# Kernel optimization log

Hardware: AMD Instinct MI355X
Metric: run time of the kernel (lower is better)

## Reference

```python
import jax, jax.numpy as jnp
import numpy as np

POS_DIM, COND_DIM, VIEW_DIM, HID = 3, 64, 3, 128
N_DENSITY, N_COLOR, SKIP = 8, 3, 4
DIN = POS_DIM + COND_DIM            # 67, density input dim
CIN = HID + VIEW_DIM                # 131, color input dim


def setup_inputs() -> dict:
    key = jax.random.key(0)
    ks = iter(jax.random.split(key, 64))

    def w(shape):
        return jax.random.normal(next(ks), shape, dtype=jnp.float32) * 0.05

    inp = {
        "pos": jax.random.normal(next(ks), (2048, 128, POS_DIM), dtype=jnp.float32),
        "cond": jax.random.normal(next(ks), (COND_DIM,), dtype=jnp.float32),
        "view": jax.random.normal(next(ks), (2048, VIEW_DIM), dtype=jnp.float32),
    }
    # density trunk: layer 0 takes DIN; layer SKIP+1 takes HID+DIN (skip concat); rest HID
    d_ins = [DIN] + [HID + DIN if i == SKIP + 1 else HID for i in range(1, N_DENSITY)]
    for i, din in enumerate(d_ins):
        inp[f"dW{i}"] = w((din, HID))
        inp[f"db{i}"] = w((HID,))
    inp["sW"], inp["sb"] = w((HID, 1)), w((1,))
    # color trunk
    c_ins = [CIN] + [HID // 2] * (N_COLOR - 1)
    for i, cin in enumerate(c_ins):
        inp[f"cW{i}"] = w((cin, HID // 2))
        inp[f"cb{i}"] = w((HID // 2,))
    inp["rW"], inp["rb"] = w((HID // 2, 3)), w((3,))
    return inp


def reference(pos, cond, view,
              dW0, db0, dW1, db1, dW2, db2, dW3, db3,
              dW4, db4, dW5, db5, dW6, db6, dW7, db7,
              sW, sb, cW0, cb0, cW1, cb1, cW2, cb2, rW, rb):
    bs, n_sample, _ = pos.shape
    cond_e = jnp.broadcast_to(cond[None, None, :], (bs, n_sample, COND_DIM))
    view_e = jnp.broadcast_to(view[:, None, :], (bs, n_sample, VIEW_DIM))

    x0 = jnp.concatenate([pos, cond_e], axis=-1)  # [bs, n, DIN]
    dWs = [dW0, dW1, dW2, dW3, dW4, dW5, dW6, dW7]
    dbs = [db0, db1, db2, db3, db4, db5, db6, db7]

    h = x0
    for i in range(N_DENSITY):
        h = jax.nn.relu(h @ dWs[i] + dbs[i])
        if i == SKIP:
            h = jnp.concatenate([x0, h], axis=-1)  # skip concat, input first
    sigma = h @ sW + sb  # [bs, n, 1]

    h = jnp.concatenate([h, view_e], axis=-1)  # [bs, n, CIN]
    cWs, cbs = [cW0, cW1, cW2], [cb0, cb1, cb2]
    for i in range(N_COLOR):
        h = jax.nn.relu(h @ cWs[i] + cbs[i])
    rgb = h @ rW + rb  # [bs, n, 3]

    return jnp.concatenate([rgb, sigma], axis=-1)  # [bs, n, 4]
```

## Files before the change

kernel.cpp:

```cpp
#include <hip/hip_runtime.h>

typedef _Float16 f16;
typedef _Float16 f16x8 __attribute__((ext_vector_type(8)));
typedef float f32x4 __attribute__((ext_vector_type(4)));

#define WS_PARAMS 262144

struct Ptrs { const float* p[29]; };

__device__ __forceinline__ int klogf(int q) {
  return ((q >> 5) << 5) | (((q >> 2) & 1) << 4) | (((q >> 3) & 3) << 2) | (q & 3);
}

__global__ void nerf_prep(Ptrs ptrs, char* __restrict__ ws) {
  const int t = threadIdx.x;
  if (blockIdx.x == 0) {
    float* P = (float*)(ws + WS_PARAMS);
    const float* cond = ptrs.p[1];
    const float* dW0 = ptrs.p[3];  const float* db0 = ptrs.p[4];
    const float* dW5 = ptrs.p[13]; const float* db5 = ptrs.p[14];
    if (t < 128) {
      float a0 = db0[t], a5 = db5[t];
      for (int k = 0; k < 64; ++k) {
        const float c = cond[k];
        a0 += c * dW0[(3 + k) * 128 + t];
        a5 += c * dW5[(3 + k) * 128 + t];
      }
      P[t] = a0;
      P[512 + t] = a5;
      for (int k = 0; k < 3; ++k) {
        P[128 + k * 128 + t] = dW0[k * 128 + t];
        P[640 + k * 128 + t] = dW5[k * 128 + t];
      }
      P[1024 + t] = ptrs.p[6][t];
      P[1152 + t] = ptrs.p[8][t];
      P[1280 + t] = ptrs.p[10][t];
      P[1408 + t] = ptrs.p[12][t];
      P[1536 + t] = ptrs.p[16][t];
      P[1664 + t] = ptrs.p[18][t];
      P[2176 + t] = ptrs.p[19][t];
    }
    if (t < 64) {
      P[1792 + t] = ptrs.p[22][t];
      for (int k = 0; k < 3; ++k)
        P[1856 + k * 64 + t] = ptrs.p[21][(128 + k) * 64 + t];
      P[2048 + t] = ptrs.p[24][t];
      P[2112 + t] = ptrs.p[26][t];
      for (int c = 0; c < 3; ++c)
        P[2308 + c * 64 + t] = ptrs.p[27][t * 3 + c];
    }
    if (t == 0) {
      P[2304] = ptrs.p[20][0];
      P[2500] = ptrs.p[28][0];
      P[2501] = ptrs.p[28][1];
      P[2502] = ptrs.p[28][2];
    }
    if (t < 3)  P[2305 + t] = 0.f;
    if (t < 57) P[2503 + t] = 0.f;
    return;
  }
  const int e = (blockIdx.x - 1) * 256 + t;
  float v; int dst;
  if (e < 114688) {
    const int img = e >> 14, o = e & 16383;
    const int j = o & 7, lane = (o >> 3) & 63, ks = (o >> 9) & 3, T = o >> 11;
    const int kraw = ks * 32 + ((lane >> 4) << 3) + j;
    const int k = (img == 0) ? kraw : klogf(kraw);
    const int ch = T * 16 + (lane & 15);
    v = ptrs.p[5 + 2 * img][(k + (img == 4 ? 67 : 0)) * 128 + ch];
    dst = img * 32768 + (((T * 4 + ks) * 64 + lane) << 4) + (j << 1);
  } else if (e < 122880) {
    const int o = e - 114688;
    const int j = o & 7, lane = (o >> 3) & 63, ks = (o >> 9) & 3, T = o >> 11;
    const int k = klogf(ks * 32 + ((lane >> 4) << 3) + j);
    const int ch = T * 16 + (lane & 15);
    v = ptrs.p[21][k * 64 + ch];
    dst = 229376 + (((T * 4 + ks) * 64 + lane) << 4) + (j << 1);
  } else if (e < 126976) {
    const int o = e - 122880;
    const int j = o & 7, lane = (o >> 3) & 63, ks = (o >> 9) & 1, T = o >> 10;
    const int k = klogf(ks * 32 + ((lane >> 4) << 3) + j);
    const int ch = T * 16 + (lane & 15);
    v = ptrs.p[23][k * 64 + ch];
    dst = 245760 + (((T * 2 + ks) * 64 + lane) << 4) + (j << 1);
  } else {
    const int o = e - 126976;
    const int j = o & 7, lane = (o >> 3) & 63, ks = (o >> 9) & 1, T = o >> 10;
    const int k = klogf(ks * 32 + ((lane >> 4) << 3) + j);
    const int ch = T * 16 + (lane & 15);
    v = ptrs.p[25][k * 64 + ch];
    dst = 253952 + (((T * 2 + ks) * 64 + lane) << 4) + (j << 1);
  }
  *(f16*)(ws + dst) = (f16)v;
}

__device__ __forceinline__ void loadF4(f16x8* A, const char* __restrict__ img,
                                       int fragBase, int lane) {
#pragma unroll
  for (int i = 0; i < 4; ++i)
    A[i] = *(const f16x8*)(img + (((fragBase + i) * 64 + lane) << 4));
}

template<int HCT, int NKS, int INIT, int CTBASE>
__device__ __forceinline__ void qL(const f16x8 B[4][4], f32x4 acc[4][8],
                                   const f16x8* A,
                                   const float* __restrict__ P,
                                   const float px[4][3],
                                   const float* __restrict__ vw2,
                                   int biasOff, int kg, int wbase) {
#pragma unroll
  for (int ct = 0; ct < HCT; ++ct) {
    const int ochB = (CTBASE + ct) * 16 + kg * 4;
    const f32x4 bq = *(const f32x4*)(P + biasOff + ochB);
    f32x4 e0, e1, e2;
    if (INIT == 1) {
      e0 = *(const f32x4*)(P + 640 + ochB);
      e1 = *(const f32x4*)(P + 768 + ochB);
      e2 = *(const f32x4*)(P + 896 + ochB);
    } else if (INIT == 2) {
      e0 = *(const f32x4*)(P + 1856 + ochB);
      e1 = *(const f32x4*)(P + 1920 + ochB);
      e2 = *(const f32x4*)(P + 1984 + ochB);
    }
#pragma unroll
    for (int ptc = 0; ptc < 4; ++ptc) {
      f32x4 v = bq;
      if (INIT == 1)
        v += px[ptc][0] * e0 + px[ptc][1] * e1 + px[ptc][2] * e2;
      if (INIT == 2) {
        const int ray = (wbase + ptc * 16) >> 7;
        v += vw2[ray * 3] * e0 + vw2[ray * 3 + 1] * e1 + vw2[ray * 3 + 2] * e2;
      }
      acc[ptc][CTBASE + ct] = v;
    }
  }
  __builtin_amdgcn_s_setprio(1);
#pragma unroll
  for (int ct = 0; ct < HCT; ++ct)
#pragma unroll
    for (int ks = 0; ks < NKS; ++ks)
#pragma unroll
      for (int ptc = 0; ptc < 4; ++ptc)
        acc[ptc][CTBASE + ct] = __builtin_amdgcn_mfma_f32_16x16x32_f16(
            A[ct * NKS + ks], B[ptc][ks], acc[ptc][CTBASE + ct], 0, 0, 0);
  __builtin_amdgcn_s_setprio(0);
}

template<int NCT>
__device__ __forceinline__ void toB(const f32x4 acc[4][8], f16x8 B[4][4]) {
#pragma unroll
  for (int ptc = 0; ptc < 4; ++ptc)
#pragma unroll
    for (int ks = 0; ks < NCT / 2; ++ks) {
      f16x8 hb;
#pragma unroll
      for (int r = 0; r < 4; ++r) {
        hb[r]     = (f16)fmaxf(acc[ptc][2 * ks][r], 0.f);
        hb[4 + r] = (f16)fmaxf(acc[ptc][2 * ks + 1][r], 0.f);
      }
      B[ptc][ks] = hb;
    }
}

__global__ __launch_bounds__(512, 2) void nerf_main(
    const float* __restrict__ pos, const float* __restrict__ view,
    const char* __restrict__ ws, float* __restrict__ out) {
  __shared__ __align__(16) float Lp[2560 + 1536 + 16];
  const int t = threadIdx.x, lane = t & 63, w = t >> 6;
  const int c = lane & 15, kg = lane >> 4;
  const int base = blockIdx.x * 512;
  const int wbase = w * 64;
  const float* P = Lp;
  float* Lpos = Lp + 2560;
  float* Lvw = Lp + 4096;

  for (int i = t; i < 2560; i += 512) Lp[i] = ((const float*)(ws + WS_PARAMS))[i];
  for (int i = t; i < 1536; i += 512) Lpos[i] = pos[base * 3 + i];
  if (t < 12) Lvw[t] = view[(base >> 7) * 3 + t];
  __syncthreads();

  f16x8 Aa[4], Ab[4];
  loadF4(Aa, ws + 0, 0, lane);

  float px[4][3];
#pragma unroll
  for (int ptc = 0; ptc < 4; ++ptc) {
    const int lp = wbase + ptc * 16 + c;
#pragma unroll
    for (int d = 0; d < 3; ++d) px[ptc][d] = Lpos[lp * 3 + d];
  }

  f16x8 B[4][4];
#pragma unroll
  for (int ptc = 0; ptc < 4; ++ptc)
#pragma unroll
    for (int ks = 0; ks < 4; ++ks) {
      f16x8 hb;
#pragma unroll
      for (int j = 0; j < 8; ++j) {
        const int ch = ks * 32 + kg * 8 + j;
        const float v = P[ch] + px[ptc][0] * P[128 + ch] + px[ptc][1] * P[256 + ch]
                      + px[ptc][2] * P[384 + ch];
        hb[j] = (f16)fmaxf(v, 0.f);
      }
      B[ptc][ks] = hb;
    }

  f32x4 acc[4][8];

#define QCE(CTB, img_, fb, BIAS, INIT_)                                        \
  loadF4(Ab, img_, fb, lane);                                                  \
  qL<1, 4, INIT_, CTB>(B, acc, Aa, P, px, Lvw, BIAS, kg, wbase);
#define QCO(CTB, img_, fb, BIAS, INIT_)                                        \
  loadF4(Aa, img_, fb, lane);                                                  \
  qL<1, 4, INIT_, CTB>(B, acc, Ab, P, px, Lvw, BIAS, kg, wbase);
#define DLAYER(img_, imgNext, BIAS, INIT_)                                     \
  QCE(0, img_,  4, BIAS, INIT_) QCO(1, img_,  8, BIAS, INIT_)                  \
  QCE(2, img_, 12, BIAS, INIT_) QCO(3, img_, 16, BIAS, INIT_)                  \
  QCE(4, img_, 20, BIAS, INIT_) QCO(5, img_, 24, BIAS, INIT_)                  \
  QCE(6, img_, 28, BIAS, INIT_) QCO(7, imgNext, 0, BIAS, INIT_)

  DLAYER(ws +      0, ws +  32768, 1024, 0) toB<8>(acc, B);
  DLAYER(ws +  32768, ws +  65536, 1152, 0) toB<8>(acc, B);
  DLAYER(ws +  65536, ws +  98304, 1280, 0) toB<8>(acc, B);
  DLAYER(ws +  98304, ws + 131072, 1408, 0) toB<8>(acc, B);
  DLAYER(ws + 131072, ws + 163840,  512, 1) toB<8>(acc, B);
  DLAYER(ws + 163840, ws + 196608, 1536, 0) toB<8>(acc, B);
  DLAYER(ws + 196608, ws + 229376, 1664, 0)
#undef DLAYER
#undef QCE
#undef QCO

  float sig[4];
#pragma unroll
  for (int ptc = 0; ptc < 4; ++ptc) {
    float s = 0.f;
#pragma unroll
    for (int ct = 0; ct < 8; ++ct) {
      const f32x4 wq = *(const f32x4*)(P + 2176 + ct * 16 + kg * 4);
      const f32x4 a = acc[ptc][ct];
#pragma unroll
      for (int r = 0; r < 4; ++r) s += fmaxf(a[r], 0.f) * wq[r];
    }
    s += __shfl_xor(s, 16);
    s += __shfl_xor(s, 32);
    sig[ptc] = s + P[2304];
  }
  toB<8>(acc, B);

  loadF4(Ab, ws + 229376,  4, lane);
  qL<1, 4, 2, 0>(B, acc, Aa, P, px, Lvw, 1792, kg, wbase);
  loadF4(Aa, ws + 229376,  8, lane);
  qL<1, 4, 2, 1>(B, acc, Ab, P, px, Lvw, 1792, kg, wbase);
  loadF4(Ab, ws + 229376, 12, lane);
  qL<1, 4, 2, 2>(B, acc, Aa, P, px, Lvw, 1792, kg, wbase);
  loadF4(Aa, ws + 245760,  0, lane);
  qL<1, 4, 2, 3>(B, acc, Ab, P, px, Lvw, 1792, kg, wbase);
  toB<4>(acc, B);

  loadF4(Ab, ws + 245760, 4, lane);
  qL<2, 2, 0, 0>(B, acc, Aa, P, px, Lvw, 2048, kg, wbase);
  loadF4(Aa, ws + 253952, 0, lane);
  qL<2, 2, 0, 2>(B, acc, Ab, P, px, Lvw, 2048, kg, wbase);
  toB<4>(acc, B);

  loadF4(Ab, ws + 253952, 4, lane);
  qL<2, 2, 0, 0>(B, acc, Aa, P, px, Lvw, 2112, kg, wbase);
  qL<2, 2, 0, 2>(B, acc, Ab, P, px, Lvw, 2112, kg, wbase);

#pragma unroll
  for (int ptc = 0; ptc < 4; ++ptc) {
    float a0 = 0.f, a1 = 0.f, a2 = 0.f;
#pragma unroll
    for (int ct = 0; ct < 4; ++ct) {
      const int ochB = ct * 16 + kg * 4;
      const f32x4 r0 = *(const f32x4*)(P + 2308 + ochB);
      const f32x4 r1 = *(const f32x4*)(P + 2372 + ochB);
      const f32x4 r2 = *(const f32x4*)(P + 2436 + ochB);
      const f32x4 a = acc[ptc][ct];
#pragma unroll
      for (int r = 0; r < 4; ++r) {
        const float h = fmaxf(a[r], 0.f);
        a0 += h * r0[r]; a1 += h * r1[r]; a2 += h * r2[r];
      }
    }
    a0 += __shfl_xor(a0, 16); a0 += __shfl_xor(a0, 32);
    a1 += __shfl_xor(a1, 16); a1 += __shfl_xor(a1, 32);
    a2 += __shfl_xor(a2, 16); a2 += __shfl_xor(a2, 32);
    if (kg == 0) {
      float4 o;
      o.x = a0 + P[2500]; o.y = a1 + P[2501]; o.z = a2 + P[2502]; o.w = sig[ptc];
      *(float4*)(out + (base + wbase + ptc * 16 + c) * 4) = o;
    }
  }
}

extern "C" void kernel_launch(void* const* d_in, const int* in_sizes, int n_in,
                              void* d_out, int out_size, void* d_ws, size_t ws_size,
                              hipStream_t stream) {
  Ptrs ptrs;
  for (int i = 0; i < 29; ++i) ptrs.p[i] = (const float*)d_in[i];
  char* ws = (char*)d_ws;
  nerf_prep<<<513, 256, 0, stream>>>(ptrs, ws);
  nerf_main<<<512, 512, 0, stream>>>((const float*)d_in[0], (const float*)d_in[2],
                                     ws, (float*)d_out);
}
```

Baseline: 82.33 us.

## Switch MLP matmuls from 16x16x32 to 32x32x16 MFMA tiles

Reworks the weight pre-swizzle and main kernel to use 32x32x16 f16 MFMA instructions, with 32-point by 32-channel tiles, in place of 16x16x32. Each wave now handles two point tiles instead of four, and the k-permutation and accumulator-to-operand repacking are redone to fit the new fragment layout. The bias is folded into the first MFMA's accumulator input. The relu is applied after a packed round-toward-zero f16 conversion. The goal is fewer MFMA issues, larger tiles per instruction and cheaper cross-lane reductions. The cost is different register pressure and a rounding mode that differs from the previous round-to-nearest conversion.

After: 94.94 us. 15.3% more time.

```diff
diff --git a/kernel.cpp b/kernel.cpp
--- a/kernel.cpp
+++ b/kernel.cpp
@@ -2,14 +2,16 @@
 
 typedef _Float16 f16;
 typedef _Float16 f16x8 __attribute__((ext_vector_type(8)));
+typedef __fp16 hf16x2 __attribute__((ext_vector_type(2)));
 typedef float f32x4 __attribute__((ext_vector_type(4)));
+typedef float f32x16 __attribute__((ext_vector_type(16)));
 
 #define WS_PARAMS 262144
 
 struct Ptrs { const float* p[29]; };
 
-__device__ __forceinline__ int klogf(int q) {
-  return ((q >> 5) << 5) | (((q >> 2) & 1) << 4) | (((q >> 3) & 3) << 2) | (q & 3);
+__device__ __forceinline__ int klog32(int q) {
+  return (q & ~12) | ((q & 4) << 1) | ((q & 8) >> 1);
 }
 
 __global__ void nerf_prep(Ptrs ptrs, char* __restrict__ ws) {
@@ -63,102 +65,138 @@
   float v; int dst;
   if (e < 114688) {
     const int img = e >> 14, o = e & 16383;
-    const int j = o & 7, lane = (o >> 3) & 63, ks = (o >> 9) & 3, T = o >> 11;
-    const int kraw = ks * 32 + ((lane >> 4) << 3) + j;
-    const int k = (img == 0) ? kraw : klogf(kraw);
-    const int ch = T * 16 + (lane & 15);
-    v = ptrs.p[5 + 2 * img][(k + (img == 4 ? 67 : 0)) * 128 + ch];
-    dst = img * 32768 + (((T * 4 + ks) * 64 + lane) << 4) + (j << 1);
+    const int j = o & 7, lane = (o >> 3) & 63, m = (o >> 9) & 7, T = o >> 12;
+    const int kraw = m * 16 + ((lane >> 5) << 3) + j;
+    const int k = (img == 0) ? kraw : klog32(kraw);
+    const int och = T * 32 + (lane & 31);
+    v = ptrs.p[5 + 2 * img][(k + (img == 4 ? 67 : 0)) * 128 + och];
+    dst = img * 32768 + (((T * 8 + m) * 64 + lane) << 4) + (j << 1);
   } else if (e < 122880) {
     const int o = e - 114688;
-    const int j = o & 7, lane = (o >> 3) & 63, ks = (o >> 9) & 3, T = o >> 11;
-    const int k = klogf(ks * 32 + ((lane >> 4) << 3) + j);
-    const int ch = T * 16 + (lane & 15);
-    v = ptrs.p[21][k * 64 + ch];
-    dst = 229376 + (((T * 4 + ks) * 64 + lane) << 4) + (j << 1);
+    const int j = o & 7, lane = (o >> 3) & 63, m = (o >> 9) & 7, T = o >> 12;
+    const int k = klog32(m * 16 + ((lane >> 5) << 3) + j);
+    const int och = T * 32 + (lane & 31);
+    v = ptrs.p[21][k * 64 + och];
+    dst = 229376 + (((T * 8 + m) * 64 + lane) << 4) + (j << 1);
   } else if (e < 126976) {
     const int o = e - 122880;
-    const int j = o & 7, lane = (o >> 3) & 63, ks = (o >> 9) & 1, T = o >> 10;
-    const int k = klogf(ks * 32 + ((lane >> 4) << 3) + j);
-    const int ch = T * 16 + (lane & 15);
-    v = ptrs.p[23][k * 64 + ch];
-    dst = 245760 + (((T * 2 + ks) * 64 + lane) << 4) + (j << 1);
+    const int j = o & 7, lane = (o >> 3) & 63, m = (o >> 9) & 3, T = o >> 11;
+    const int k = klog32(m * 16 + ((lane >> 5) << 3) + j);
+    const int och = T * 32 + (lane & 31);
+    v = ptrs.p[23][k * 64 + och];
+    dst = 245760 + (((T * 4 + m) * 64 + lane) << 4) + (j << 1);
   } else {
     const int o = e - 126976;
-    const int j = o & 7, lane = (o >> 3) & 63, ks = (o >> 9) & 1, T = o >> 10;
-    const int k = klogf(ks * 32 + ((lane >> 4) << 3) + j);
-    const int ch = T * 16 + (lane & 15);
-    v = ptrs.p[25][k * 64 + ch];
-    dst = 253952 + (((T * 2 + ks) * 64 + lane) << 4) + (j << 1);
+    const int j = o & 7, lane = (o >> 3) & 63, m = (o >> 9) & 3, T = o >> 11;
+    const int k = klog32(m * 16 + ((lane >> 5) << 3) + j);
+    const int och = T * 32 + (lane & 31);
+    v = ptrs.p[25][k * 64 + och];
+    dst = 253952 + (((T * 4 + m) * 64 + lane) << 4) + (j << 1);
   }
   *(f16*)(ws + dst) = (f16)v;
 }
 
 __device__ __forceinline__ void loadF4(f16x8* A, const char* __restrict__ img,
-                                       int fragBase, int lane) {
+                                       int fb, int lane) {
 #pragma unroll
   for (int i = 0; i < 4; ++i)
-    A[i] = *(const f16x8*)(img + (((fragBase + i) * 64 + lane) << 4));
-}
-
-template<int HCT, int NKS, int INIT, int CTBASE>
-__device__ __forceinline__ void qL(const f16x8 B[4][4], f32x4 acc[4][8],
-                                   const f16x8* A,
-                                   const float* __restrict__ P,
-                                   const float px[4][3],
-                                   const float* __restrict__ vw2,
-                                   int biasOff, int kg, int wbase) {
-#pragma unroll
-  for (int ct = 0; ct < HCT; ++ct) {
-    const int ochB = (CTBASE + ct) * 16 + kg * 4;
-    const f32x4 bq = *(const f32x4*)(P + biasOff + ochB);
-    f32x4 e0, e1, e2;
+    A[i] = *(const f16x8*)(img + (((fb + i) * 64 + lane) << 4));
+}
+
+__device__ __forceinline__ f16x8 packRelu(const f32x4 v0, const f32x4 v1) {
+  const hf16x2 p0 = __builtin_amdgcn_cvt_pkrtz(v0[0], v0[1]);
+  const hf16x2 p1 = __builtin_amdgcn_cvt_pkrtz(v0[2], v0[3]);
+  const hf16x2 p2 = __builtin_amdgcn_cvt_pkrtz(v1[0], v1[1]);
+  const hf16x2 p3 = __builtin_amdgcn_cvt_pkrtz(v1[2], v1[3]);
+  f16x8 hb;
+  hb[0] = (f16)p0[0]; hb[1] = (f16)p0[1]; hb[2] = (f16)p1[0]; hb[3] = (f16)p1[1];
+  hb[4] = (f16)p2[0]; hb[5] = (f16)p2[1]; hb[6] = (f16)p3[0]; hb[7] = (f16)p3[1];
+#pragma unroll
+  for (int e2 = 0; e2 < 8; ++e2)
+    hb[e2] = hb[e2] > (f16)0.f ? hb[e2] : (f16)0.f;
+  return hb;
+}
+
+template<int T, int KH, int INIT>
+__device__ __forceinline__ void qL32(const f16x8 B[2][8], f32x16 acc[2][4],
+                                     const f16x8* A, const float* __restrict__ P,
+                                     const float px[2][3],
+                                     const float* __restrict__ vw2,
+                                     int biasOff, int h4, int wbase) {
+  if (KH == 0) {
+    f32x4 bq[4];
+#pragma unroll
+    for (int q = 0; q < 4; ++q)
+      bq[q] = *(const f32x4*)(P + biasOff + T * 32 + q * 8 + h4);
+    f32x4 e0[4], e1[4], e2[4];
     if (INIT == 1) {
-      e0 = *(const f32x4*)(P + 640 + ochB);
-      e1 = *(const f32x4*)(P + 768 + ochB);
-      e2 = *(const f32x4*)(P + 896 + ochB);
+#pragma unroll
+      for (int q = 0; q < 4; ++q) {
+        e0[q] = *(const f32x4*)(P + 640 + T * 32 + q * 8 + h4);
+        e1[q] = *(const f32x4*)(P + 768 + T * 32 + q * 8 + h4);
+        e2[q] = *(const f32x4*)(P + 896 + T * 32 + q * 8 + h4);
+      }
     } else if (INIT == 2) {
-      e0 = *(const f32x4*)(P + 1856 + ochB);
-      e1 = *(const f32x4*)(P + 1920 + ochB);
-      e2 = *(const f32x4*)(P + 1984 + ochB);
-    }
-#pragma unroll
-    for (int ptc = 0; ptc < 4; ++ptc) {
-      f32x4 v = bq;
-      if (INIT == 1)
-        v += px[ptc][0] * e0 + px[ptc][1] * e1 + px[ptc][2] * e2;
-      if (INIT == 2) {
-        const int ray = (wbase + ptc * 16) >> 7;
-        v += vw2[ray * 3] * e0 + vw2[ray * 3 + 1] * e1 + vw2[ray * 3 + 2] * e2;
-      }
-      acc[ptc][CTBASE + ct] = v;
-    }
-  }
-  __builtin_amdgcn_s_setprio(1);
-#pragma unroll
-  for (int ct = 0; ct < HCT; ++ct)
-#pragma unroll
-    for (int ks = 0; ks < NKS; ++ks)
-#pragma unroll
-      for (int ptc = 0; ptc < 4; ++ptc)
-        acc[ptc][CTBASE + ct] = __builtin_amdgcn_mfma_f32_16x16x32_f16(
-            A[ct * NKS + ks], B[ptc][ks], acc[ptc][CTBASE + ct], 0, 0, 0);
-  __builtin_amdgcn_s_setprio(0);
-}
-
-template<int NCT>
-__device__ __forceinline__ void toB(const f32x4 acc[4][8], f16x8 B[4][4]) {
-#pragma unroll
-  for (int ptc = 0; ptc < 4; ++ptc)
-#pragma unroll
-    for (int ks = 0; ks < NCT / 2; ++ks) {
-      f16x8 hb;
-#pragma unroll
-      for (int r = 0; r < 4; ++r) {
-        hb[r]     = (f16)fmaxf(acc[ptc][2 * ks][r], 0.f);
-        hb[4 + r] = (f16)fmaxf(acc[ptc][2 * ks + 1][r], 0.f);
-      }
-      B[ptc][ks] = hb;
+#pragma unroll
+      for (int q = 0; q < 4; ++q) {
+        e0[q] = *(const f32x4*)(P + 1856 + T * 32 + q * 8 + h4);
+        e1[q] = *(const f32x4*)(P + 1920 + T * 32 + q * 8 + h4);
+        e2[q] = *(const f32x4*)(P + 1984 + T * 32 + q * 8 + h4);
+      }
+    }
+    __builtin_amdgcn_s_setprio(1);
+#pragma unroll
+    for (int pt = 0; pt < 2; ++pt) {
+      f32x16 s;
+#pragma unroll
+      for (int q = 0; q < 4; ++q) {
+        f32x4 vq = bq[q];
+        if (INIT == 1)
+          vq += px[pt][0] * e0[q] + px[pt][1] * e1[q] + px[pt][2] * e2[q];
+        if (INIT == 2) {
+          const int ray = (wbase + pt * 32) >> 7;
+          vq += vw2[ray * 3] * e0[q] + vw2[ray * 3 + 1] * e1[q]
+              + vw2[ray * 3 + 2] * e2[q];
+        }
+#pragma unroll
+        for (int e3 = 0; e3 < 4; ++e3) s[q * 4 + e3] = vq[e3];
+      }
+      acc[pt][T] = __builtin_amdgcn_mfma_f32_32x32x16_f16(A[0], B[pt][KH * 4 + 0],
+                                                          s, 0, 0, 0);
+    }
+#pragma unroll
+    for (int i = 1; i < 4; ++i)
+#pragma unroll
+      for (int pt = 0; pt < 2; ++pt)
+        acc[pt][T] = __builtin_amdgcn_mfma_f32_32x32x16_f16(
+            A[i], B[pt][KH * 4 + i], acc[pt][T], 0, 0, 0);
+    __builtin_amdgcn_s_setprio(0);
+  } else {
+    __builtin_amdgcn_s_setprio(1);
+#pragma unroll
+    for (int i = 0; i < 4; ++i)
+#pragma unroll
+      for (int pt = 0; pt < 2; ++pt)
+        acc[pt][T] = __builtin_amdgcn_mfma_f32_32x32x16_f16(
+            A[i], B[pt][KH * 4 + i], acc[pt][T], 0, 0, 0);
+    __builtin_amdgcn_s_setprio(0);
+  }
+}
+
+template<int NM>
+__device__ __forceinline__ void toB32(const f32x16 acc[2][4], f16x8 B[2][8]) {
+#pragma unroll
+  for (int pt = 0; pt < 2; ++pt)
+#pragma unroll
+    for (int m = 0; m < NM; ++m) {
+      const int s = (m & 1) * 8;
+      f32x4 v0, v1;
+#pragma unroll
+      for (int e3 = 0; e3 < 4; ++e3) {
+        v0[e3] = acc[pt][m >> 1][s + e3];
+        v1[e3] = acc[pt][m >> 1][s + 4 + e3];
+      }
+      B[pt][m] = packRelu(v0, v1);
     }
 }
 
@@ -167,7 +205,8 @@
     const char* __restrict__ ws, float* __restrict__ out) {
   __shared__ __align__(16) float Lp[2560 + 1536 + 16];
   const int t = threadIdx.x, lane = t & 63, w = t >> 6;
-  const int c = lane & 15, kg = lane >> 4;
+  const int c32 = lane & 31;
+  const int h4 = ((lane >> 5) << 2), h8 = ((lane >> 5) << 3);
   const int base = blockIdx.x * 512;
   const int wbase = w * 64;
   const float* P = Lp;
@@ -182,115 +221,117 @@
   f16x8 Aa[4], Ab[4];
   loadF4(Aa, ws + 0, 0, lane);
 
-  float px[4][3];
-#pragma unroll
-  for (int ptc = 0; ptc < 4; ++ptc) {
-    const int lp = wbase + ptc * 16 + c;
-#pragma unroll
-    for (int d = 0; d < 3; ++d) px[ptc][d] = Lpos[lp * 3 + d];
-  }
-
-  f16x8 B[4][4];
-#pragma unroll
-  for (int ptc = 0; ptc < 4; ++ptc)
-#pragma unroll
-    for (int ks = 0; ks < 4; ++ks) {
-      f16x8 hb;
-#pragma unroll
-      for (int j = 0; j < 8; ++j) {
-        const int ch = ks * 32 + kg * 8 + j;
-        const float v = P[ch] + px[ptc][0] * P[128 + ch] + px[ptc][1] * P[256 + ch]
-                      + px[ptc][2] * P[384 + ch];
-        hb[j] = (f16)fmaxf(v, 0.f);
-      }
-      B[ptc][ks] = hb;
-    }
-
-  f32x4 acc[4][8];
-
-#define QCE(CTB, img_, fb, BIAS, INIT_)                                        \
+  float px[2][3];
+#pragma unroll
+  for (int pt = 0; pt < 2; ++pt) {
+    const int lp = wbase + pt * 32 + c32;
+#pragma unroll
+    for (int d = 0; d < 3; ++d) px[pt][d] = Lpos[lp * 3 + d];
+  }
+
+  f16x8 B[2][8];
+#pragma unroll
+  for (int m = 0; m < 8; ++m) {
+    const int chb = m * 16 + h8;
+    const f32x4 b0  = *(const f32x4*)(P + chb),       b1  = *(const f32x4*)(P + chb + 4);
+    const f32x4 w00 = *(const f32x4*)(P + 128 + chb), w01 = *(const f32x4*)(P + 128 + chb + 4);
+    const f32x4 w10 = *(const f32x4*)(P + 256 + chb), w11 = *(const f32x4*)(P + 256 + chb + 4);
+    const f32x4 w20 = *(const f32x4*)(P + 384 + chb), w21 = *(const f32x4*)(P + 384 + chb + 4);
+#pragma unroll
+    for (int pt = 0; pt < 2; ++pt) {
+      const f32x4 v0 = b0 + px[pt][0] * w00 + px[pt][1] * w10 + px[pt][2] * w20;
+      const f32x4 v1 = b1 + px[pt][0] * w01 + px[pt][1] * w11 + px[pt][2] * w21;
+      B[pt][m] = packRelu(v0, v1);
+    }
+  }
+
+  f32x16 acc[2][4];
+
+#define QCE(T_, KH_, img_, fb, BIAS, INIT_)                                    \
   loadF4(Ab, img_, fb, lane);                                                  \
-  qL<1, 4, INIT_, CTB>(B, acc, Aa, P, px, Lvw, BIAS, kg, wbase);
-#define QCO(CTB, img_, fb, BIAS, INIT_)                                        \
+  qL32<T_, KH_, INIT_>(B, acc, Aa, P, px, Lvw, BIAS, h4, wbase);
+#define QCO(T_, KH_, img_, fb, BIAS, INIT_)                                    \
   loadF4(Aa, img_, fb, lane);                                                  \
-  qL<1, 4, INIT_, CTB>(B, acc, Ab, P, px, Lvw, BIAS, kg, wbase);
+  qL32<T_, KH_, INIT_>(B, acc, Ab, P, px, Lvw, BIAS, h4, wbase);
 #define DLAYER(img_, imgNext, BIAS, INIT_)                                     \
-  QCE(0, img_,  4, BIAS, INIT_) QCO(1, img_,  8, BIAS, INIT_)                  \
-  QCE(2, img_, 12, BIAS, INIT_) QCO(3, img_, 16, BIAS, INIT_)                  \
-  QCE(4, img_, 20, BIAS, INIT_) QCO(5, img_, 24, BIAS, INIT_)                  \
-  QCE(6, img_, 28, BIAS, INIT_) QCO(7, imgNext, 0, BIAS, INIT_)
-
-  DLAYER(ws +      0, ws +  32768, 1024, 0) toB<8>(acc, B);
-  DLAYER(ws +  32768, ws +  65536, 1152, 0) toB<8>(acc, B);
-  DLAYER(ws +  65536, ws +  98304, 1280, 0) toB<8>(acc, B);
-  DLAYER(ws +  98304, ws + 131072, 1408, 0) toB<8>(acc, B);
-  DLAYER(ws + 131072, ws + 163840,  512, 1) toB<8>(acc, B);
-  DLAYER(ws + 163840, ws + 196608, 1536, 0) toB<8>(acc, B);
+  QCE(0, 0, img_,  4, BIAS, INIT_) QCO(0, 1, img_,  8, BIAS, INIT_)            \
+  QCE(1, 0, img_, 12, BIAS, INIT_) QCO(1, 1, img_, 16, BIAS, INIT_)            \
+  QCE(2, 0, img_, 20, BIAS, INIT_) QCO(2, 1, img_, 24, BIAS, INIT_)            \
+  QCE(3, 0, img_, 28, BIAS, INIT_) QCO(3, 1, imgNext, 0, BIAS, INIT_)
+
+  DLAYER(ws +      0, ws +  32768, 1024, 0) toB32<8>(acc, B);
+  DLAYER(ws +  32768, ws +  65536, 1152, 0) toB32<8>(acc, B);
+  DLAYER(ws +  65536, ws +  98304, 1280, 0) toB32<8>(acc, B);
+  DLAYER(ws +  98304, ws + 131072, 1408, 0) toB32<8>(acc, B);
+  DLAYER(ws + 131072, ws + 163840,  512, 1) toB32<8>(acc, B);
+  DLAYER(ws + 163840, ws + 196608, 1536, 0) toB32<8>(acc, B);
   DLAYER(ws + 196608, ws + 229376, 1664, 0)
 #undef DLAYER
 #undef QCE
 #undef QCO
 
-  float sig[4];
-#pragma unroll
-  for (int ptc = 0; ptc < 4; ++ptc) {
+  float sig[2];
+#pragma unroll
+  for (int pt = 0; pt < 2; ++pt) {
     float s = 0.f;
 #pragma unroll
-    for (int ct = 0; ct < 8; ++ct) {
-      const f32x4 wq = *(const f32x4*)(P + 2176 + ct * 16 + kg * 4);
-      const f32x4 a = acc[ptc][ct];
-#pragma unroll
-      for (int r = 0; r < 4; ++r) s += fmaxf(a[r], 0.f) * wq[r];
-    }
-    s += __shfl_xor(s, 16);
+    for (int T = 0; T < 4; ++T)
+#pragma unroll
+      for (int q = 0; q < 4; ++q) {
+        const f32x4 wq = *(const f32x4*)(P + 2176 + T * 32 + q * 8 + h4);
+#pragma unroll
+        for (int e3 = 0; e3 < 4; ++e3)
+          s += fmaxf(acc[pt][T][q * 4 + e3], 0.f) * wq[e3];
+      }
     s += __shfl_xor(s, 32);
-    sig[ptc] = s + P[2304];
-  }
-  toB<8>(acc, B);
+    sig[pt] = s + P[2304];
+  }
+  toB32<8>(acc, B);
 
   loadF4(Ab, ws + 229376,  4, lane);
-  qL<1, 4, 2, 0>(B, acc, Aa, P, px, Lvw, 1792, kg, wbase);
+  qL32<0, 0, 2>(B, acc, Aa, P, px, Lvw, 1792, h4, wbase);
   loadF4(Aa, ws + 229376,  8, lane);
-  qL<1, 4, 2, 1>(B, acc, Ab, P, px, Lvw, 1792, kg, wbase);
+  qL32<0, 1, 2>(B, acc, Ab, P, px, Lvw, 1792, h4, wbase);
   loadF4(Ab, ws + 229376, 12, lane);
-  qL<1, 4, 2, 2>(B, acc, Aa, P, px, Lvw, 1792, kg, wbase);
+  qL32<1, 0, 2>(B, acc, Aa, P, px, Lvw, 1792, h4, wbase);
   loadF4(Aa, ws + 245760,  0, lane);
-  qL<1, 4, 2, 3>(B, acc, Ab, P, px, Lvw, 1792, kg, wbase);
-  toB<4>(acc, B);
+  qL32<1, 1, 2>(B, acc, Ab, P, px, Lvw, 1792, h4, wbase);
+  toB32<4>(acc, B);
 
   loadF4(Ab, ws + 245760, 4, lane);
-  qL<2, 2, 0, 0>(B, acc, Aa, P, px, Lvw, 2048, kg, wbase);
+  qL32<0, 0, 0>(B, acc, Aa, P, px, Lvw, 2048, h4, wbase);
   loadF4(Aa, ws + 253952, 0, lane);
-  qL<2, 2, 0, 2>(B, acc, Ab, P, px, Lvw, 2048, kg, wbase);
-  toB<4>(acc, B);
+  qL32<1, 0, 0>(B, acc, Ab, P, px, Lvw, 2048, h4, wbase);
+  toB32<4>(acc, B);
 
   loadF4(Ab, ws + 253952, 4, lane);
-  qL<2, 2, 0, 0>(B, acc, Aa, P, px, Lvw, 2112, kg, wbase);
-  qL<2, 2, 0, 2>(B, acc, Ab, P, px, Lvw, 2112, kg, wbase);
-
-#pragma unroll
-  for (int ptc = 0; ptc < 4; ++ptc) {
+  qL32<0, 0, 0>(B, acc, Aa, P, px, Lvw, 2112, h4, wbase);
+  qL32<1, 0, 0>(B, acc, Ab, P, px, Lvw, 2112, h4, wbase);
+
+#pragma unroll
+  for (int pt = 0; pt < 2; ++pt) {
     float a0 = 0.f, a1 = 0.f, a2 = 0.f;
 #pragma unroll
-    for (int ct = 0; ct < 4; ++ct) {
-      const int ochB = ct * 16 + kg * 4;
-      const f32x4 r0 = *(const f32x4*)(P + 2308 + ochB);
-      const f32x4 r1 = *(const f32x4*)(P + 2372 + ochB);
-      const f32x4 r2 = *(const f32x4*)(P + 2436 + ochB);
-      const f32x4 a = acc[ptc][ct];
-#pragma unroll
-      for (int r = 0; r < 4; ++r) {
-        const float h = fmaxf(a[r], 0.f);
-        a0 += h * r0[r]; a1 += h * r1[r]; a2 += h * r2[r];
-      }
-    }
-    a0 += __shfl_xor(a0, 16); a0 += __shfl_xor(a0, 32);
-    a1 += __shfl_xor(a1, 16); a1 += __shfl_xor(a1, 32);
-    a2 += __shfl_xor(a2, 16); a2 += __shfl_xor(a2, 32);
-    if (kg == 0) {
+    for (int T = 0; T < 2; ++T)
+#pragma unroll
+      for (int q = 0; q < 4; ++q) {
+        const int ob = T * 32 + q * 8 + h4;
+        const f32x4 r0 = *(const f32x4*)(P + 2308 + ob);
+        const f32x4 r1 = *(const f32x4*)(P + 2372 + ob);
+        const f32x4 r2 = *(const f32x4*)(P + 2436 + ob);
+#pragma unroll
+        for (int e3 = 0; e3 < 4; ++e3) {
+          const float h = fmaxf(acc[pt][T][q * 4 + e3], 0.f);
+          a0 += h * r0[e3]; a1 += h * r1[e3]; a2 += h * r2[e3];
+        }
+      }
+    a0 += __shfl_xor(a0, 32);
+    a1 += __shfl_xor(a1, 32);
+    a2 += __shfl_xor(a2, 32);
+    if (lane < 32) {
       float4 o;
-      o.x = a0 + P[2500]; o.y = a1 + P[2501]; o.z = a2 + P[2502]; o.w = sig[ptc];
-      *(float4*)(out + (base + wbase + ptc * 16 + c) * 4) = o;
+      o.x = a0 + P[2500]; o.y = a1 + P[2501]; o.z = a2 + P[2502]; o.w = sig[pt];
+      *(float4*)(out + (base + wbase + pt * 32 + c32) * 4) = o;
     }
   }
 }
```
